# Performance work log

Measured on AMD Instinct MI355X. Metric: run time of the kernel, lower is better.

## Reference

```python
import jax, jax.numpy as jnp
import numpy as np


def setup_inputs() -> dict:
    key = jax.random.key(0)
    ks = jax.random.split(key, 8)
    B, L, K = 32, 1024, 256
    s = lambda k, shape, sc: jax.random.normal(k, shape, dtype=jnp.float32) * sc
    return {
        "x": s(ks[0], (B, L, K), 1.0),
        "rWx": s(ks[1], (K, 4 * K), 0.05),   # reader LSTM kernel
        "rWh": s(ks[2], (K, 4 * K), 0.05),   # reader recurrent kernel
        "rb": jnp.zeros((4 * K,), jnp.float32),
        "wWx": s(ks[3], (2 * K, 4 * K), 0.05),  # writer LSTM kernel (input dim 2K)
        "wWh": s(ks[4], (K, 4 * K), 0.05),
        "wb": jnp.zeros((4 * K,), jnp.float32),
        "cW": s(ks[5], (2 * K, 2 * K), 0.05),    # composer Dense(2K), linear activation
        "cb": jnp.zeros((2 * K,), jnp.float32),
    }


def _lstm(x_t, h, c, Wx, Wh, b):
    # Keras LSTM: gate order i, f, g(candidate), o; sigmoid recurrent activation, tanh activation
    gates = x_t @ Wx + h @ Wh + b
    i, f, g, o = jnp.split(gates, 4, axis=-1)
    c_new = jax.nn.sigmoid(f) * c + jax.nn.sigmoid(i) * jnp.tanh(g)
    h_new = jax.nn.sigmoid(o) * jnp.tanh(c_new)
    return h_new, c_new


def reference(x, rWx, rWh, rb, wWx, wWh, wb, cW, cb):
    B, L, K = x.shape
    zeros = jnp.zeros((B, K), x.dtype)
    # mem_0 = input (get_initial_state copies input to mem_0); LSTM states start at zero
    carry0 = (zeros, zeros, x, zeros, zeros)  # (hr, cr, mem, hw, cw)

    def step(carry, x_t):
        hr, cr, mem, hw, cw = carry
        # Eq 1: reader LSTM -> o_t
        hr, cr = _lstm(x_t, hr, cr, rWx, rWh, rb)  # o_t = hr, (B, K)
        # Eq 2-3: attention over memory
        z_t = jax.nn.softmax(jnp.einsum('bk,blk->bl', hr, mem), axis=-1)  # (B, L)
        m_rt = jnp.einsum('bl,blk->bk', z_t, mem)                          # (B, K)
        # Eq 4: composer (linear Dense on concat)
        c_t = jnp.concatenate([hr, m_rt], axis=-1) @ cW + cb               # (B, 2K)
        # Eq 5: writer LSTM -> h_t
        hw, cw = _lstm(c_t, hw, cw, wWx, wWh, wb)                          # (B, K)
        # Eq 6: memory update (selective forget + add)
        mem = mem * (1.0 - z_t[..., None]) + hw[:, None, :] * z_t[..., None]
        return (hr, cr, mem, hw, cw), hw

    _, hs = jax.lax.scan(step, carry0, jnp.swapaxes(x, 0, 1))
    # return_mode='all_outputs': full sequence of writer outputs
    return jnp.swapaxes(hs, 0, 1)  # (B, L, K)
```

## Files before the change

kernel.cpp:

```cpp
#include <hip/hip_runtime.h>
#include <math.h>


#define Bb 32
#define LL 1024
#define KK 256
#define AR 776
#define ASCOPE __HIP_MEMORY_SCOPE_AGENT
#define FSTR 16

__device__ __forceinline__ float sigf(float v) { return 1.0f / (1.0f + __expf(-v)); }

__device__ __forceinline__ void st_coh2(float* p, float a, float b) {
    float2 v = make_float2(a, b);
    __hip_atomic_store((unsigned long long*)p,
                       __builtin_bit_cast(unsigned long long, v),
                       __ATOMIC_RELAXED, ASCOPE);
}
__device__ __forceinline__ float2 ld_coh2(const float* p) {
    unsigned long long u = __hip_atomic_load((const unsigned long long*)p,
                                             __ATOMIC_RELAXED, ASCOPE);
    return __builtin_bit_cast(float2, u);
}

__device__ __forceinline__ void bar_arrive(unsigned* fown, unsigned val) {
    asm volatile("s_waitcnt vmcnt(0) lgkmcnt(0)" ::: "memory");
    __syncthreads();
    if (threadIdx.x == 0)
        __hip_atomic_store(fown, val, __ATOMIC_RELAXED, ASCOPE);
}
__device__ __forceinline__ void bar_wait(unsigned* fbase, unsigned val) {
    if (threadIdx.x < 64) {
        for (;;) {
            unsigned v = __hip_atomic_load(fbase + threadIdx.x * FSTR,
                                           __ATOMIC_RELAXED, ASCOPE);
            if (__all(v >= val)) break;
            __builtin_amdgcn_s_sleep(1);
        }
    }
    asm volatile("" ::: "memory");
    __syncthreads();
}

__global__ __launch_bounds__(256) void k_pre(
    const float* __restrict__ cW, const float* __restrict__ cb,
    const float* __restrict__ wWx, const float* __restrict__ wb,
    const float* __restrict__ rWx, const float* __restrict__ rWh,
    const float* __restrict__ wWh,
    float* __restrict__ WfT, float* __restrict__ rWT, float* __restrict__ bfv,
    unsigned* __restrict__ flg) {
    int bid = blockIdx.x, tid = threadIdx.x;
    if (bid < 512) {
        __shared__ float srow[512];
        srow[tid] = cW[(size_t)bid * 512 + tid];
        srow[256 + tid] = cW[(size_t)bid * 512 + 256 + tid];
        __syncthreads();
#pragma unroll
        for (int rep = 0; rep < 4; rep++) {
            int col = rep * 256 + tid;
            float a = 0.f;
#pragma unroll 4
            for (int c = 0; c < 512; c++) a += srow[c] * wWx[(size_t)c * 1024 + col];
            WfT[(size_t)col * 768 + bid] = a;
        }
    } else if (bid < 516) {
        int col = (bid - 512) * 256 + tid;
        float a = wb[col];
#pragma unroll 4
        for (int c = 0; c < 512; c++) a += cb[c] * wWx[(size_t)c * 1024 + col];
        bfv[col] = a;
    } else if (bid < 644) {
        int k0 = (bid - 516) * 2;
        for (int kk = k0; kk < k0 + 2; kk++)
            for (int col = tid; col < 1024; col += 256)
                rWT[(size_t)col * 512 + kk] = rWx[(size_t)kk * 1024 + col];
    } else if (bid < 772) {
        int k0 = (bid - 644) * 2;
        for (int kk = k0; kk < k0 + 2; kk++)
            for (int col = tid; col < 1024; col += 256)
                rWT[(size_t)col * 512 + 256 + kk] = rWh[(size_t)kk * 1024 + col];
    } else if (bid < 900) {
        int k0 = (bid - 772) * 2;
        for (int kk = k0; kk < k0 + 2; kk++)
            for (int col = tid; col < 1024; col += 256)
                WfT[(size_t)col * 768 + 512 + kk] = wWh[(size_t)kk * 1024 + col];
    } else {
        int idx = (bid - 900) * 256 + tid;
        flg[idx] = 0u;
    }
}

__global__ __launch_bounds__(512, 1) void k_nse(
    const float* __restrict__ x, const float* __restrict__ rb,
    const float* __restrict__ rWT, const float* __restrict__ WfT,
    const float* __restrict__ bfv, float* __restrict__ st,
    float* __restrict__ out, unsigned* __restrict__ flg) {
    __shared__ float smem[32768 + 8 * AR + 8 + 8 + 16 + 128 + 128 + 128];
    float* memT   = smem;
    float* arena  = smem + 32768;
    float* sMw    = arena + 8 * AR;
    float* sSw    = sMw + 8;
    float* sMS    = sSw + 8;
    float* sScore = sMS + 16;
    float* sGr    = sScore + 128;
    float* sGw    = sGr + 128;

    float* hrb[2] = { st, st + 8192 };
    float* hwb[2] = { st + 16384, st + 24576 };
    float* partMS = st + 32832;
    float* partV  = st + 33344;

    int g = blockIdx.x, tid = threadIdx.x;
    int w = tid >> 6, ln = tid & 63;
    int bA = g >> 3;
    int bg = g >> 6, gl = g & 63;
    int j0 = gl * 4;
    unsigned* fA = flg + (bg * 64) * FSTR;
    unsigned* fB = flg + (256 + bg * 64) * FSTR;
    unsigned* fAo = fA + gl * FSTR;
    unsigned* fBo = fB + gl * FSTR;

    int bln = ln & 7, ks = (ln >> 3) & 3, cp = ln >> 5;
    int c = 2 * w + cp;
    int gate = c >> 2, jlc = c & 3;
    int col = gate * KK + j0 + jlc;
    int bglw = bg * 8 + w;

    const float4* wfc = (const float4*)(WfT + (size_t)col * 768);
    const float4* rwc = (const float4*)(rWT + (size_t)col * 512);
    float4 w2[16];
#pragma unroll
    for (int i = 0; i < 16; i++) w2[i] = wfc[64 + ks * 16 + ((i + 3 * ks) & 15)];

    float crreg = 0.f, cwreg = 0.f;

    const float4* xsrc = (const float4*)(x + ((size_t)bA * LL + (size_t)(g & 7) * 128) * KK);
#pragma unroll
    for (int i = 0; i < 16; i++) ((float4*)memT)[tid + i * 512] = xsrc[tid + i * 512];
    ((float4*)(arena + w * AR))[ln] = ((const float4*)(x + (size_t)bglw * LL * KK))[ln];
    ((float4*)(arena + w * AR + 256))[ln] = make_float4(0.f, 0.f, 0.f, 0.f);
    __syncthreads();
    {
        float accr = 0.f;
        const float4* ain = (const float4*)(arena + bln * AR);
#pragma unroll 8
        for (int i = 0; i < 32; i++) {
            int idx = ks * 32 + ((i + 5 * ks) & 31);
            float4 a = ain[idx], q = rwc[idx];
            accr += a.x * q.x + a.y * q.y + a.z * q.z + a.w * q.w;
        }
        accr += __shfl_xor(accr, 8);
        accr += __shfl_xor(accr, 16);
        if (!(ln & 24)) sGr[c * 8 + bln] = accr + rb[col];
    }
    __syncthreads();
    if (tid < 32) {
        int pb = tid & 7, pj = tid >> 3;
        int bgp = bg * 8 + pb;
        float gi = sGr[(0 + pj) * 8 + pb], gG = sGr[(8 + pj) * 8 + pb];
        float go = sGr[(12 + pj) * 8 + pb];
        float cn = sigf(gi) * tanhf(gG);
        float hn = sigf(go) * tanhf(cn);
        crreg = cn;
        float hn2 = __shfl(hn, tid + 8);
        if (!(pj & 1)) st_coh2(hrb[0] + bgp * KK + j0 + pj, hn, hn2);
    }
    bar_arrive(fBo, 1u);
    float4 xreg = ((const float4*)(x + ((size_t)bglw * LL + 1) * KK))[ln];
    bar_wait(fB, 1u);

    for (int t = 0; t < LL; t++) {
        int cur = t & 1, prv = cur ^ 1;
        const float* hp = hrb[cur] + bA * KK + ln * 4;
        float2 ha = ld_coh2(hp), hc = ld_coh2(hp + 2);
        float4 h4 = make_float4(ha.x, ha.y, hc.x, hc.y);
        float4 hrs2, hws2, w4 = make_float4(0.f, 0.f, 0.f, 0.f);
        {
            const float* hq = hrb[cur] + bglw * KK + ln * 4;
            float2 a = ld_coh2(hq), cc = ld_coh2(hq + 2);
            hrs2 = make_float4(a.x, a.y, cc.x, cc.y);
        }
        float Mprev = 0.f, invS = 0.f;
        if (t > 0) {
            const float* wp0 = hwb[prv] + bA * KK + ln * 4;
            float2 wa = ld_coh2(wp0), wc = ld_coh2(wp0 + 2);
            w4 = make_float4(wa.x, wa.y, wc.x, wc.y);
            const float* hq = hwb[prv] + bglw * KK + ln * 4;
            float2 a = ld_coh2(hq), cc = ld_coh2(hq + 2);
            hws2 = make_float4(a.x, a.y, cc.x, cc.y);
            Mprev = sMS[(bA & 7) * 2];
            invS = 1.0f / sMS[(bA & 7) * 2 + 1];
        } else {
            hws2 = make_float4(0.f, 0.f, 0.f, 0.f);
        }
        float dp[16];
        float* rowp = memT + w * 16 * KK;
        if (t > 0) {
            float scs[16];
            const float4* sp = (const float4*)(sScore + w * 16);
#pragma unroll
            for (int q2 = 0; q2 < 4; q2++) {
                float4 s4 = sp[q2];
                scs[q2 * 4 + 0] = s4.x; scs[q2 * 4 + 1] = s4.y;
                scs[q2 * 4 + 2] = s4.z; scs[q2 * 4 + 3] = s4.w;
            }
#pragma unroll
            for (int i = 0; i < 16; i++) {
                float4* vp = (float4*)(rowp + i * KK) + ln;
                float4 v = *vp;
                float z = __expf(scs[i] - Mprev) * invS;
                float om = 1.0f - z;
                v.x = v.x * om + w4.x * z;
                v.y = v.y * om + w4.y * z;
                v.z = v.z * om + w4.z * z;
                v.w = v.w * om + w4.w * z;
                *vp = v;
                dp[i] = h4.x * v.x + h4.y * v.y + h4.z * v.z + h4.w * v.w;
            }
        } else {
#pragma unroll
            for (int i = 0; i < 16; i++) {
                float4 v = *((float4*)(rowp + i * KK) + ln);
                dp[i] = h4.x * v.x + h4.y * v.y + h4.z * v.z + h4.w * v.w;
            }
        }
        {
            float* sT = arena + w * AR;
            int rr = ln >> 3, kk2 = ln & 7;
#pragma unroll
            for (int hh = 0; hh < 2; hh++) {
                int o = hh * 8;
#pragma unroll
                for (int j = 0; j < 8; j++) sT[ln * 9 + j] = dp[o + j];
                float ps = 0.f;
#pragma unroll
                for (int j = 0; j < 8; j++) ps += sT[(j * 8 + kk2) * 9 + rr];
                ps += __shfl_xor(ps, 1);
                ps += __shfl_xor(ps, 2);
                ps += __shfl_xor(ps, 4);
                if (kk2 == 0) sScore[w * 16 + o + rr] = ps;
            }
        }
        {
            float scs2[16];
            const float4* sp = (const float4*)(sScore + w * 16);
#pragma unroll
            for (int q2 = 0; q2 < 4; q2++) {
                float4 s4 = sp[q2];
                scs2[q2 * 4 + 0] = s4.x; scs2[q2 * 4 + 1] = s4.y;
                scs2[q2 * 4 + 2] = s4.z; scs2[q2 * 4 + 3] = s4.w;
            }
            float M16 = scs2[0];
#pragma unroll
            for (int i = 1; i < 16; i++) M16 = fmaxf(M16, scs2[i]);
            float Sw = 0.f;
            float4 Vw = make_float4(0.f, 0.f, 0.f, 0.f);
#pragma unroll
            for (int i = 0; i < 16; i++) {
                float e = __expf(scs2[i] - M16);
                Sw += e;
                float4 v = *((float4*)(rowp + i * KK) + ln);
                Vw.x += e * v.x; Vw.y += e * v.y; Vw.z += e * v.z; Vw.w += e * v.w;
            }
            ((float4*)(arena + w * AR))[ln] = Vw;
            if (ln == 0) { sMw[w] = M16; sSw[w] = Sw; }
        }
        __syncthreads();
        if (tid < 128) {
            float M = sMw[0];
#pragma unroll
            for (int q2 = 1; q2 < 8; q2++) M = fmaxf(M, sMw[q2]);
            float S = 0.f, V0 = 0.f, V1 = 0.f;
#pragma unroll
            for (int q2 = 0; q2 < 8; q2++) {
                float e = __expf(sMw[q2] - M);
                S += e * sSw[q2];
                V0 += e * arena[q2 * AR + 2 * tid];
                V1 += e * arena[q2 * AR + 2 * tid + 1];
            }
            st_coh2(partV + (size_t)g * KK + 2 * tid, V0, V1);
            if (tid == 0) st_coh2(partMS + g * 2, M, S);
        }
        bar_arrive(fAo, (unsigned)(t + 1));

        if (t + 1 < LL) ((float4*)(arena + w * AR))[ln] = xreg;
        ((float4*)(arena + w * AR + 256))[ln] = hrs2;
        ((float4*)(arena + w * AR + 512))[ln] = hws2;
        __syncthreads();

        float accw = (ks == 0) ? bfv[col] : 0.f;
        {
            const float4* ain = (const float4*)(arena + bln * AR);
#pragma unroll 8
            for (int i = 0; i < 16; i++) {
                int idx = ks * 16 + ((i + 3 * ks) & 15);
                float4 a = ain[64 + idx], q = wfc[idx];
                accw += a.x * q.x + a.y * q.y + a.z * q.z + a.w * q.w;
            }
#pragma unroll 8
            for (int i = 0; i < 16; i++) {
                int idx = ks * 16 + ((i + 3 * ks) & 15);
                float4 a = ain[128 + idx], q = wfc[128 + idx];
                accw += a.x * q.x + a.y * q.y + a.z * q.z + a.w * q.w;
            }
        }
        if (t + 1 < LL) {
            float accr = 0.f;
            const float4* ain = (const float4*)(arena + bln * AR);
#pragma unroll 8
            for (int i = 0; i < 32; i++) {
                int idx = ks * 32 + ((i + 5 * ks) & 31);
                float4 a = ain[idx], q = rwc[idx];
                accr += a.x * q.x + a.y * q.y + a.z * q.z + a.w * q.w;
            }
            accr += __shfl_xor(accr, 8);
            accr += __shfl_xor(accr, 16);
            if (!(ln & 24)) sGr[c * 8 + bln] = accr + rb[col];
        }
        __syncthreads();

        {
            unsigned tgt = (unsigned)(t + 1);
            for (;;) {
                unsigned v = tgt;
                if (ln < 8)
                    v = __hip_atomic_load(fA + (8 * w + ln) * FSTR, __ATOMIC_RELAXED, ASCOPE);
                if (__all(v >= tgt)) break;
                __builtin_amdgcn_s_sleep(1);
            }
        }
        {
            float2 pms[8];
            float2 pva[8], pvb[8];
#pragma unroll
            for (int q2 = 0; q2 < 8; q2++) {
                int src = bg * 64 + w * 8 + q2;
                pms[q2] = ld_coh2(partMS + src * 2);
                const float* pv = partV + (size_t)src * KK + ln * 4;
                pva[q2] = ld_coh2(pv);
                pvb[q2] = ld_coh2(pv + 2);
            }
            float M = pms[0].x;
#pragma unroll
            for (int q2 = 1; q2 < 8; q2++) M = fmaxf(M, pms[q2].x);
            float S = 0.f;
            float4 V = make_float4(0.f, 0.f, 0.f, 0.f);
#pragma unroll
            for (int q2 = 0; q2 < 8; q2++) {
                float e = __expf(pms[q2].x - M);
                S += e * pms[q2].y;
                V.x += e * pva[q2].x; V.y += e * pva[q2].y;
                V.z += e * pvb[q2].x; V.w += e * pvb[q2].y;
            }
            float rS = 1.0f / S;
            ((float4*)(arena + w * AR))[ln] =
                make_float4(V.x * rS, V.y * rS, V.z * rS, V.w * rS);
            if (ln == 0) { sMS[w * 2] = M; sMS[w * 2 + 1] = S; }
        }
        __syncthreads();

        {
            const float4* ain = (const float4*)(arena + bln * AR);
#pragma unroll
            for (int i = 0; i < 16; i++) {
                int idx = ks * 16 + ((i + 3 * ks) & 15);
                float4 a = ain[idx];
                accw += a.x * w2[i].x + a.y * w2[i].y + a.z * w2[i].z + a.w * w2[i].w;
            }
            accw += __shfl_xor(accw, 8);
            accw += __shfl_xor(accw, 16);
            if (!(ln & 24)) sGw[c * 8 + bln] = accw;
        }
        __syncthreads();

        if (tid < 32) {
            int pb = tid & 7, pj = tid >> 3;
            int bgp = bg * 8 + pb;
            if (t + 1 < LL) {
                float gi = sGr[(0 + pj) * 8 + pb], gf = sGr[(4 + pj) * 8 + pb];
                float gG = sGr[(8 + pj) * 8 + pb], go = sGr[(12 + pj) * 8 + pb];
                float cn = sigf(gf) * crreg + sigf(gi) * tanhf(gG);
                float hn = sigf(go) * tanhf(cn);
                crreg = cn;
                float hn2 = __shfl(hn, tid + 8);
                if (!(pj & 1)) st_coh2(hrb[prv] + bgp * KK + j0 + pj, hn, hn2);
            }
            {
                float gi = sGw[(0 + pj) * 8 + pb], gf = sGw[(4 + pj) * 8 + pb];
                float gG = sGw[(8 + pj) * 8 + pb], go = sGw[(12 + pj) * 8 + pb];
                float cp2 = (t > 0) ? cwreg : 0.f;
                float cn = sigf(gf) * cp2 + sigf(gi) * tanhf(gG);
                float hn = sigf(go) * tanhf(cn);
                cwreg = cn;
                float hn2 = __shfl(hn, tid + 8);
                if (!(pj & 1)) {
                    st_coh2(hwb[cur] + bgp * KK + j0 + pj, hn, hn2);
                    *(float2*)(out + ((size_t)bgp * LL + t) * KK + j0 + pj) =
                        make_float2(hn, hn2);
                }
            }
        }
        bar_arrive(fBo, (unsigned)(t + 2));
        if (t + 2 < LL)
            xreg = ((const float4*)(x + ((size_t)bglw * LL + (size_t)(t + 2)) * KK))[ln];
        bar_wait(fB, (unsigned)(t + 2));
    }
}

extern "C" void kernel_launch(void* const* d_in, const int* in_sizes, int n_in,
                              void* d_out, int out_size, void* d_ws, size_t ws_size,
                              hipStream_t stream) {
    const float* x   = (const float*)d_in[0];
    const float* rWx = (const float*)d_in[1];
    const float* rWh = (const float*)d_in[2];
    const float* rb  = (const float*)d_in[3];
    const float* wWx = (const float*)d_in[4];
    const float* wWh = (const float*)d_in[5];
    const float* wb  = (const float*)d_in[6];
    const float* cW  = (const float*)d_in[7];
    const float* cb  = (const float*)d_in[8];
    float* out = (float*)d_out;

    float* ws = (float*)d_ws;
    float* WfT = ws;
    float* rWT = ws + 786432;
    float* bfv = ws + 786432 + 524288;
    float* st  = bfv + 1024;
    unsigned* flg = (unsigned*)(st + 98880);

    k_pre<<<932, 256, 0, stream>>>(cW, cb, wWx, wb, rWx, rWh, wWh, WfT, rWT, bfv, flg);

    const float* a_x = x; const float* a_rb = rb;
    const float* a_rWT = rWT; const float* a_WfT = WfT; const float* a_bf = bfv;
    float* a_st = st; float* a_out = out; unsigned* a_flg = flg;
    void* args[] = { &a_x, &a_rb, &a_rWT, &a_WfT, &a_bf, &a_st, &a_out, &a_flg };
    hipLaunchCooperativeKernel(reinterpret_cast<void*>(k_nse), dim3(256), dim3(512),
                               args, 0, stream);
}
```

Before: 13.15 ms.

## Keep LSTM weight columns in registers and reduce over all 8 batches per lane

Changes how the per-step gate dot products are split across lanes. Before, each lane handled one batch row and a quarter of K, reading weights from global memory each step. Now each lane holds its slice of the reader and writer weight columns in registers, loaded once, and accumulates all 8 batch rows, followed by a 5-level shuffle reduction and a select. This removes repeated global weight loads inside the time loop. In exchange it raises register pressure and adds more shuffle and LDS broadcast traffic, and the arena offsets are re-indexed to match.

```diff
diff --git a/kernel.cpp b/kernel.cpp
--- a/kernel.cpp
+++ b/kernel.cpp
@@ -10,6 +10,9 @@
 #define FSTR 16
 
 __device__ __forceinline__ float sigf(float v) { return 1.0f / (1.0f + __expf(-v)); }
+__device__ __forceinline__ float dot4(float4 a, float4 b) {
+    return a.x * b.x + a.y * b.y + a.z * b.z + a.w * b.w;
+}
 
 __device__ __forceinline__ void st_coh2(float* p, float a, float b) {
     float2 v = make_float2(a, b);
@@ -120,17 +123,20 @@
     unsigned* fAo = fA + gl * FSTR;
     unsigned* fBo = fB + gl * FSTR;
 
-    int bln = ln & 7, ks = (ln >> 3) & 3, cp = ln >> 5;
+    int kq = ln & 31, cp = ln >> 5;
     int c = 2 * w + cp;
     int gate = c >> 2, jlc = c & 3;
     int col = gate * KK + j0 + jlc;
     int bglw = bg * 8 + w;
 
-    const float4* wfc = (const float4*)(WfT + (size_t)col * 768);
-    const float4* rwc = (const float4*)(rWT + (size_t)col * 512);
-    float4 w2[16];
-#pragma unroll
-    for (int i = 0; i < 16; i++) w2[i] = wfc[64 + ks * 16 + ((i + 3 * ks) & 15)];
+    const float4* wfp = (const float4*)(WfT + (size_t)col * 768);
+    const float4* rwp = (const float4*)(rWT + (size_t)col * 512);
+    float4 ww0 = wfp[kq],       ww1 = wfp[32 + kq];
+    float4 ww2 = wfp[64 + kq],  ww3 = wfp[96 + kq];
+    float4 ww4 = wfp[128 + kq], ww5 = wfp[160 + kq];
+    float4 wr0 = rwp[kq],       wr1 = rwp[32 + kq];
+    float4 wr2 = rwp[64 + kq],  wr3 = rwp[96 + kq];
+    float rbc = rb[col], bfc = bfv[col];
 
     float crreg = 0.f, cwreg = 0.f;
 
@@ -138,20 +144,27 @@
 #pragma unroll
     for (int i = 0; i < 16; i++) ((float4*)memT)[tid + i * 512] = xsrc[tid + i * 512];
     ((float4*)(arena + w * AR))[ln] = ((const float4*)(x + (size_t)bglw * LL * KK))[ln];
-    ((float4*)(arena + w * AR + 256))[ln] = make_float4(0.f, 0.f, 0.f, 0.f);
+    ((float4*)(arena + w * AR))[64 + ln] = make_float4(0.f, 0.f, 0.f, 0.f);
     __syncthreads();
     {
-        float accr = 0.f;
-        const float4* ain = (const float4*)(arena + bln * AR);
-#pragma unroll 8
-        for (int i = 0; i < 32; i++) {
-            int idx = ks * 32 + ((i + 5 * ks) & 31);
-            float4 a = ain[idx], q = rwc[idx];
-            accr += a.x * q.x + a.y * q.y + a.z * q.z + a.w * q.w;
-        }
-        accr += __shfl_xor(accr, 8);
-        accr += __shfl_xor(accr, 16);
-        if (!(ln & 24)) sGr[c * 8 + bln] = accr + rb[col];
+        float accr[8];
+#pragma unroll
+        for (int b = 0; b < 8; b++) {
+            const float4* ain = (const float4*)(arena + b * AR);
+            accr[b] = dot4(ain[kq], wr0) + dot4(ain[32 + kq], wr1)
+                    + dot4(ain[64 + kq], wr2) + dot4(ain[96 + kq], wr3);
+        }
+#pragma unroll
+        for (int m = 1; m <= 16; m <<= 1)
+#pragma unroll
+            for (int b = 0; b < 8; b++) accr[b] += __shfl_xor(accr[b], m);
+        if ((ln & 31) < 8) {
+            int bsel = ln & 7;
+            float v = accr[0];
+#pragma unroll
+            for (int q = 1; q < 8; q++) v = (bsel == q) ? accr[q] : v;
+            sGr[c * 8 + bsel] = v + rbc;
+        }
     }
     __syncthreads();
     if (tid < 32) {
@@ -284,38 +297,36 @@
         bar_arrive(fAo, (unsigned)(t + 1));
 
         if (t + 1 < LL) ((float4*)(arena + w * AR))[ln] = xreg;
-        ((float4*)(arena + w * AR + 256))[ln] = hrs2;
-        ((float4*)(arena + w * AR + 512))[ln] = hws2;
-        __syncthreads();
-
-        float accw = (ks == 0) ? bfv[col] : 0.f;
-        {
-            const float4* ain = (const float4*)(arena + bln * AR);
-#pragma unroll 8
-            for (int i = 0; i < 16; i++) {
-                int idx = ks * 16 + ((i + 3 * ks) & 15);
-                float4 a = ain[64 + idx], q = wfc[idx];
-                accw += a.x * q.x + a.y * q.y + a.z * q.z + a.w * q.w;
-            }
-#pragma unroll 8
-            for (int i = 0; i < 16; i++) {
-                int idx = ks * 16 + ((i + 3 * ks) & 15);
-                float4 a = ain[128 + idx], q = wfc[128 + idx];
-                accw += a.x * q.x + a.y * q.y + a.z * q.z + a.w * q.w;
-            }
+        ((float4*)(arena + w * AR))[64 + ln] = hrs2;
+        ((float4*)(arena + w * AR))[128 + ln] = hws2;
+        __syncthreads();
+
+        float accw[8];
+#pragma unroll
+        for (int b = 0; b < 8; b++) {
+            const float4* ain = (const float4*)(arena + b * AR);
+            accw[b] = dot4(ain[64 + kq], ww0) + dot4(ain[96 + kq], ww1)
+                    + dot4(ain[128 + kq], ww4) + dot4(ain[160 + kq], ww5);
         }
         if (t + 1 < LL) {
-            float accr = 0.f;
-            const float4* ain = (const float4*)(arena + bln * AR);
-#pragma unroll 8
-            for (int i = 0; i < 32; i++) {
-                int idx = ks * 32 + ((i + 5 * ks) & 31);
-                float4 a = ain[idx], q = rwc[idx];
-                accr += a.x * q.x + a.y * q.y + a.z * q.z + a.w * q.w;
-            }
-            accr += __shfl_xor(accr, 8);
-            accr += __shfl_xor(accr, 16);
-            if (!(ln & 24)) sGr[c * 8 + bln] = accr + rb[col];
+            float accr[8];
+#pragma unroll
+            for (int b = 0; b < 8; b++) {
+                const float4* ain = (const float4*)(arena + b * AR);
+                accr[b] = dot4(ain[kq], wr0) + dot4(ain[32 + kq], wr1)
+                        + dot4(ain[64 + kq], wr2) + dot4(ain[96 + kq], wr3);
+            }
+#pragma unroll
+            for (int m = 1; m <= 16; m <<= 1)
+#pragma unroll
+                for (int b = 0; b < 8; b++) accr[b] += __shfl_xor(accr[b], m);
+            if ((ln & 31) < 8) {
+                int bsel = ln & 7;
+                float v = accr[0];
+#pragma unroll
+                for (int q = 1; q < 8; q++) v = (bsel == q) ? accr[q] : v;
+                sGr[c * 8 + bsel] = v + rbc;
+            }
         }
         __syncthreads();
 
@@ -360,16 +371,22 @@
         __syncthreads();
 
         {
-            const float4* ain = (const float4*)(arena + bln * AR);
-#pragma unroll
-            for (int i = 0; i < 16; i++) {
-                int idx = ks * 16 + ((i + 3 * ks) & 15);
-                float4 a = ain[idx];
-                accw += a.x * w2[i].x + a.y * w2[i].y + a.z * w2[i].z + a.w * w2[i].w;
-            }
-            accw += __shfl_xor(accw, 8);
-            accw += __shfl_xor(accw, 16);
-            if (!(ln & 24)) sGw[c * 8 + bln] = accw;
+#pragma unroll
+            for (int b = 0; b < 8; b++) {
+                const float4* ain = (const float4*)(arena + b * AR);
+                accw[b] += dot4(ain[kq], ww2) + dot4(ain[32 + kq], ww3);
+            }
+#pragma unroll
+            for (int m = 1; m <= 16; m <<= 1)
+#pragma unroll
+                for (int b = 0; b < 8; b++) accw[b] += __shfl_xor(accw[b], m);
+            if ((ln & 31) < 8) {
+                int bsel = ln & 7;
+                float v = accw[0];
+#pragma unroll
+                for (int q = 1; q < 8; q++) v = (bsel == q) ? accw[q] : v;
+                sGw[c * 8 + bsel] = v + bfc;
+            }
         }
         __syncthreads();
 
```

After: 34.45 ms. +161.9%, slower.
